# Kernel optimization log

Measured on AMD Instinct MI355X. Metric: run time of the kernel, lower is better.

The kernel has to match this reference:

```python
import jax, jax.numpy as jnp
import numpy as np

N = 20000
E = 320000
F_IN = 50
HID = 64          # hidden_channels
HEADS = 8
WIDTH = HID * HEADS  # 512
NUM_CLASSES = 121


def setup_inputs() -> dict:
    key = jax.random.key(0)
    ks = jax.random.split(key, 16)
    def p(k, shape, fan_in):
        return (jax.random.normal(k, shape, dtype=jnp.float32) / np.sqrt(fan_in)).astype(jnp.float32)
    x = jax.random.normal(ks[0], (N, F_IN), dtype=jnp.float32)
    edge_index = jax.random.randint(ks[1], (2, E), 0, N, dtype=jnp.int64)
    return {
        "x": x,
        "edge_index": edge_index,
        # layer 1: 50 -> 64, heads=8, concat
        "W1": p(ks[2], (F_IN, HEADS * HID), F_IN),
        "a1_src": p(ks[3], (HEADS, HID), HID),
        "a1_dst": p(ks[4], (HEADS, HID), HID),
        "b1": jnp.zeros((HEADS * HID,), jnp.float32),
        # layer 2: 512 -> 512, heads=1, concat
        "W2": p(ks[5], (WIDTH, WIDTH), WIDTH),
        "a2_src": p(ks[6], (1, WIDTH), WIDTH),
        "a2_dst": p(ks[7], (1, WIDTH), WIDTH),
        "b2": jnp.zeros((WIDTH,), jnp.float32),
        # layer 3: 512 -> 121, heads=1, concat=False (mean)
        "W3": p(ks[8], (WIDTH, NUM_CLASSES), WIDTH),
        "a3_src": p(ks[9], (1, NUM_CLASSES), NUM_CLASSES),
        "a3_dst": p(ks[10], (1, NUM_CLASSES), NUM_CLASSES),
        "b3": jnp.zeros((NUM_CLASSES,), jnp.float32),
    }


def gat_conv(x, src, dst, W, a_src, a_dst, b, heads, out_ch, concat):
    n = x.shape[0]
    h = (x @ W).reshape(n, heads, out_ch)                 # [N, H, C]
    al_s = jnp.sum(h * a_src, axis=-1)                     # [N, H]
    al_d = jnp.sum(h * a_dst, axis=-1)                     # [N, H]
    e = jax.nn.leaky_relu(al_s[src] + al_d[dst], 0.2)      # [E, H]
    # edge softmax per destination node (stable)
    m = jax.ops.segment_max(e, dst, num_segments=n)        # [N, H]
    m = jnp.where(jnp.isfinite(m), m, 0.0)
    ex = jnp.exp(e - m[dst])
    z = jax.ops.segment_sum(ex, dst, num_segments=n)       # [N, H]
    alpha = ex / (z[dst] + 1e-16)                          # [E, H]
    msg = h[src] * alpha[..., None]                        # [E, H, C]
    out = jax.ops.segment_sum(msg, dst, num_segments=n)    # [N, H, C]
    out = out.reshape(n, heads * out_ch) if concat else out.mean(axis=1)
    return out + b


def reference(x, edge_index, W1, a1_src, a1_dst, b1, W2, a2_src, a2_dst, b2, W3, a3_src, a3_dst, b3):
    n = x.shape[0]
    # PyG GATConv adds self loops by default
    loops = jnp.arange(n, dtype=edge_index.dtype)
    src = jnp.concatenate([edge_index[0], loops])
    dst = jnp.concatenate([edge_index[1], loops])
    # eval mode: dropout is identity
    x1 = gat_conv(x, src, dst, W1, a1_src, a1_dst, b1, HEADS, HID, True)
    h = jax.nn.elu(x1)
    x1 = gat_conv(h, src, dst, W2, a2_src, a2_dst, b2, 1, WIDTH, True)
    h = jax.nn.elu(x1)
    x1 = gat_conv(h, src, dst, W3, a3_src, a3_dst, b3, 1, NUM_CLASSES, False)
    return x1
```

## Files before the change

### kernel.cpp

```cpp
#include <hip/hip_runtime.h>
#include <hip/hip_bf16.h>
#include <hip/hip_fp16.h>

#define NN     20000
#define ERAW   320000
#define ETOT   (ERAW + NN)
#define F_IN   50
#define HID    64
#define HEADS  8
#define WIDTH  512
#define NCLS   121
#define NCLS_P 128

typedef __attribute__((ext_vector_type(8))) __bf16 bf16x8;
typedef __attribute__((ext_vector_type(4))) float floatx4;

__device__ __forceinline__ unsigned short f32_to_bf16_rn(float f) {
  unsigned u = __float_as_uint(f);
  unsigned r = u + 0x7fffu + ((u >> 16) & 1u);
  return (unsigned short)(r >> 16);
}
__device__ __forceinline__ void split_one(float f, unsigned short& h,
                                          unsigned short& l) {
  h = f32_to_bf16_rn(f);
  float fh = __uint_as_float(((unsigned)h) << 16);
  l = f32_to_bf16_rn(f - fh);
}

__device__ __forceinline__ float2 u2f2(unsigned u) {
  __half2 hv = *reinterpret_cast<__half2*>(&u);
  return __half22float2(hv);
}

__device__ __forceinline__ void gll16(const unsigned short* g,
                                      const unsigned short* l) {
  __builtin_amdgcn_global_load_lds(
      (const __attribute__((address_space(1))) unsigned int*)(const void*)g,
      (__attribute__((address_space(3))) unsigned int*)(void*)l, 16, 0, 0);
}

#define PW_BLOCKS 449
__global__ __launch_bounds__(256) void prep_weights(
    const float* __restrict__ W1, const float* __restrict__ W2,
    const float* __restrict__ W3, const float* __restrict__ a1s,
    const float* __restrict__ a1d, unsigned short* __restrict__ w1hHi,
    unsigned short* __restrict__ w1hLo, unsigned short* __restrict__ w2tHi,
    unsigned short* __restrict__ w2tLo, unsigned short* __restrict__ w3tHi,
    unsigned short* __restrict__ w3tLo, float* __restrict__ w1as,
    float* __restrict__ w1ad) {
  __shared__ float t[32][33];
  const int b = blockIdx.x;
  if (b < 320) {
    const float* W;
    unsigned short *thi, *tlo;
    int M, Mp, bx, by;
    const int K = WIDTH;
    if (b < 256) {
      W = W2; thi = w2tHi; tlo = w2tLo; M = WIDTH; Mp = WIDTH;
      bx = b & 15; by = b >> 4;
    } else {
      int bb = b - 256;
      W = W3; thi = w3tHi; tlo = w3tLo; M = NCLS; Mp = NCLS_P;
      bx = bb & 15; by = bb >> 4;
    }
    int k0 = bx * 32, m0 = by * 32;
    int tx = threadIdx.x & 31, ty = threadIdx.x >> 5;
    #pragma unroll
    for (int r = 0; r < 4; ++r) {
      int k = k0 + ty + r * 8, m = m0 + tx;
      float v = 0.f;
      if (k < K && m < M) v = W[(size_t)k * M + m];
      t[ty + r * 8][tx] = v;
    }
    __syncthreads();
    #pragma unroll
    for (int r = 0; r < 4; ++r) {
      int m = m0 + ty + r * 8, k = k0 + tx;
      if (m < Mp && k < K) {
        unsigned short h, l;
        split_one(t[tx][ty + r * 8], h, l);
        thi[(size_t)m * K + k] = h;
        tlo[(size_t)m * K + k] = l;
      }
    }
  } else if (b < 448) {
    int idx = (b - 320) * 256 + threadIdx.x;
    if (idx < HEADS * HID * HID) {
      int hd = idx >> 12, rem = idx & 4095;
      int col = rem >> 6, k = rem & 63;
      float v = (k < F_IN) ? W1[(size_t)k * WIDTH + hd * HID + col] : 0.f;
      unsigned short h, l;
      split_one(v, h, l);
      w1hHi[idx] = h;
      w1hLo[idx] = l;
    }
  } else {
    for (int idx = threadIdx.x; idx < 2 * F_IN * HEADS; idx += 256) {
      int which = idx >= F_IN * HEADS;
      int r = which ? idx - F_IN * HEADS : idx;
      int k = r >> 3, h = r & 7;
      const float* a = which ? a1d : a1s;
      float s = 0.f;
      for (int c = 0; c < HID; ++c)
        s += W1[(size_t)k * WIDTH + h * HID + c] * a[h * HID + c];
      (which ? w1ad : w1as)[r] = s;
    }
  }
}

template <int MI>
__global__ __launch_bounds__(512) void gemm_split_db(
    const unsigned short* __restrict__ Ahi, const unsigned short* __restrict__ Alo,
    const unsigned short* __restrict__ Bthi, const unsigned short* __restrict__ Btlo,
    __half* __restrict__ C16, int N, int K, int M, int Mp, int RB, int CB) {
  constexpr int ABUF = MI * 2048;
  constexpr int BHALF = MI * 4096;
  constexpr int BUF = MI * 4096 + 16384;
  constexpr int NGW = (MI * 8 + 32) / 8;
  __shared__ unsigned short lds[2 * BUF];

  const int f = blockIdx.x;
  const int xcd = f & 7;
  const int g = f >> 3;
  const int cb = g % CB;
  const int rb = (g / CB) * 8 + xcd;
  if (rb >= RB) return;
  const int r0 = rb * (MI * 32), c0 = cb * 128;

  const int tid = threadIdx.x;
  const int wave = tid >> 6, lane = tid & 63;
  const int wr = wave >> 2, wc = wave & 3;
  const int lkg = lane >> 4, lmn = lane & 15;

  const int row8 = lane >> 3, cslot = lane & 7;
  const unsigned short* gsrc[NGW];
  int ldsoff[NGW];
  #pragma unroll
  for (int i = 0; i < NGW; ++i) {
    int q = wave * NGW + i;
    int a, rg;
    if (q < MI * 4)      { a = 0; rg = q; }
    else if (q < MI * 8) { a = 1; rg = q - MI * 4; }
    else { int qb = q - MI * 8; a = 2 + (qb >> 4); rg = qb & 15; }
    int r = rg * 8 + row8;
    int c = cslot ^ (r & 7);
    const unsigned short* base =
        (a == 0) ? Ahi : (a == 1) ? Alo : (a == 2) ? Bthi : Btlo;
    size_t grow;
    if (a < 2) {
      int ra = r0 + r;
      if (ra > N - 1) ra = N - 1;
      grow = (size_t)ra;
    } else {
      grow = (size_t)(c0 + r);
    }
    gsrc[i] = base + grow * K + c * 8;
    int aoff = (a == 0) ? 0 : (a == 1) ? ABUF : (a == 2) ? BHALF
                                              : (BHALF + 8192);
    ldsoff[i] = aoff + rg * 512;
  }

  int rowA[MI], m7A[MI], rowB[2], m7B[2];
  #pragma unroll
  for (int mi = 0; mi < MI; ++mi) {
    int m = wr * (MI * 16) + mi * 16 + lmn;
    rowA[mi] = m * 64;  m7A[mi] = m & 7;
  }
  #pragma unroll
  for (int ni = 0; ni < 2; ++ni) {
    int n = wc * 32 + ni * 16 + lmn;
    rowB[ni] = BHALF + n * 64;  m7B[ni] = n & 7;
  }

  floatx4 acc[MI][2] = {};

  #pragma unroll
  for (int i = 0; i < NGW; ++i) gll16(gsrc[i], lds + ldsoff[i]);

  const int nk = K >> 6;
  for (int t = 0; t < nk; ++t) {
    if (t + 1 < nk) {
      const unsigned short* dst = lds + ((t + 1) & 1) * BUF;
      #pragma unroll
      for (int i = 0; i < NGW; ++i)
        gll16(gsrc[i] + (t + 1) * 64, dst + ldsoff[i]);
      if constexpr (MI == 4) {
        asm volatile("s_waitcnt vmcnt(8)" ::: "memory");
      } else {
        asm volatile("s_waitcnt vmcnt(6)" ::: "memory");
      }
    } else {
      asm volatile("s_waitcnt vmcnt(0)" ::: "memory");
    }
    __builtin_amdgcn_sched_barrier(0);
    __builtin_amdgcn_s_barrier();
    __builtin_amdgcn_sched_barrier(0);

    const unsigned short* Lb = lds + (t & 1) * BUF;
    #pragma unroll
    for (int ksub = 0; ksub < 2; ++ksub) {
      bf16x8 fAhi[MI], fAlo[MI], fBhi[2], fBlo[2];
      #pragma unroll
      for (int mi = 0; mi < MI; ++mi) {
        int s = rowA[mi] + (((ksub << 2) | lkg) ^ m7A[mi]) * 8;
        fAhi[mi] = *(const bf16x8*)(Lb + s);
        fAlo[mi] = *(const bf16x8*)(Lb + s + ABUF);
      }
      #pragma unroll
      for (int ni = 0; ni < 2; ++ni) {
        int s = rowB[ni] + (((ksub << 2) | lkg) ^ m7B[ni]) * 8;
        fBhi[ni] = *(const bf16x8*)(Lb + s);
        fBlo[ni] = *(const bf16x8*)(Lb + s + 8192);
      }
      #pragma unroll
      for (int mi = 0; mi < MI; ++mi)
        #pragma unroll
        for (int ni = 0; ni < 2; ++ni) {
          acc[mi][ni] = __builtin_amdgcn_mfma_f32_16x16x32_bf16(
              fAhi[mi], fBhi[ni], acc[mi][ni], 0, 0, 0);
          acc[mi][ni] = __builtin_amdgcn_mfma_f32_16x16x32_bf16(
              fAhi[mi], fBlo[ni], acc[mi][ni], 0, 0, 0);
          acc[mi][ni] = __builtin_amdgcn_mfma_f32_16x16x32_bf16(
              fAlo[mi], fBhi[ni], acc[mi][ni], 0, 0, 0);
        }
    }

    __builtin_amdgcn_sched_barrier(0);
    asm volatile("s_waitcnt lgkmcnt(0)" ::: "memory");
    __builtin_amdgcn_s_barrier();
    __builtin_amdgcn_sched_barrier(0);
  }

  #pragma unroll
  for (int mi = 0; mi < MI; ++mi) {
    #pragma unroll
    for (int r = 0; r < 4; ++r) {
      int grow = r0 + wr * (MI * 16) + mi * 16 + lkg * 4 + r;
      if (grow >= N) continue;
      #pragma unroll
      for (int ni = 0; ni < 2; ++ni) {
        int gcol = c0 + wc * 32 + ni * 16 + lmn;
        float v = (gcol < M) ? acc[mi][ni][r] : 0.f;
        C16[(size_t)grow * Mp + gcol] = __float2half(v);
      }
    }
  }
}

__global__ __launch_bounds__(256) void gemm_l1_heads(
    const unsigned short* __restrict__ Ahi, const unsigned short* __restrict__ Alo,
    const unsigned short* __restrict__ Bthi, const unsigned short* __restrict__ Btlo,
    unsigned short* __restrict__ outHi, unsigned short* __restrict__ outLo,
    const float* __restrict__ bias) {
  __shared__ unsigned short sAhi[8192], sAlo[8192], sBhi[4096], sBlo[4096];
  const int tid = threadIdx.x;
  const int wave = tid >> 6, lane = tid & 63;
  const int r0 = blockIdx.x * 128;
  const int hd = blockIdx.y;
  const int lkg = lane >> 4, lmn = lane & 15;

  #pragma unroll
  for (int t = 0; t < 4; ++t) {
    int cid = tid + t * 256;
    int row = cid >> 3, c = cid & 7;
    int gr = r0 + row; if (gr > NN - 1) gr = NN - 1;
    const size_t goff = (size_t)gr * WIDTH + hd * HID + c * 8;
    int loff = (((c >> 2) * 4 + (c & 3)) * 128 + row) * 8;
    *(uint4*)(sAhi + loff) = *(const uint4*)(Ahi + goff);
    *(uint4*)(sAlo + loff) = *(const uint4*)(Alo + goff);
  }
  #pragma unroll
  for (int t = 0; t < 2; ++t) {
    int cid = tid + t * 256;
    int col = cid >> 3, c = cid & 7;
    const size_t goff = (size_t)(hd * HID + col) * HID + c * 8;
    int loff = (((c >> 2) * 4 + (c & 3)) * 64 + col) * 8;
    *(uint4*)(sBhi + loff) = *(const uint4*)(Bthi + goff);
    *(uint4*)(sBlo + loff) = *(const uint4*)(Btlo + goff);
  }
  __syncthreads();

  floatx4 acc[2][4] = {};
  #pragma unroll
  for (int ks = 0; ks < 2; ++ks) {
    bf16x8 fAhi[2], fAlo[2], fBhi[4], fBlo[4];
    #pragma unroll
    for (int mi = 0; mi < 2; ++mi) {
      int m = wave * 32 + mi * 16 + lmn;
      int off = ((ks * 4 + lkg) * 128 + m) * 8;
      fAhi[mi] = *(const bf16x8*)(sAhi + off);
      fAlo[mi] = *(const bf16x8*)(sAlo + off);
    }
    #pragma unroll
    for (int ni = 0; ni < 4; ++ni) {
      int n = ni * 16 + lmn;
      int off = ((ks * 4 + lkg) * 64 + n) * 8;
      fBhi[ni] = *(const bf16x8*)(sBhi + off);
      fBlo[ni] = *(const bf16x8*)(sBlo + off);
    }
    #pragma unroll
    for (int mi = 0; mi < 2; ++mi)
      #pragma unroll
      for (int ni = 0; ni < 4; ++ni) {
        acc[mi][ni] = __builtin_amdgcn_mfma_f32_16x16x32_bf16(
            fAhi[mi], fBhi[ni], acc[mi][ni], 0, 0, 0);
        acc[mi][ni] = __builtin_amdgcn_mfma_f32_16x16x32_bf16(
            fAhi[mi], fBlo[ni], acc[mi][ni], 0, 0, 0);
        acc[mi][ni] = __builtin_amdgcn_mfma_f32_16x16x32_bf16(
            fAlo[mi], fBhi[ni], acc[mi][ni], 0, 0, 0);
      }
  }

  #pragma unroll
  for (int mi = 0; mi < 2; ++mi) {
    #pragma unroll
    for (int r = 0; r < 4; ++r) {
      int grow = r0 + wave * 32 + mi * 16 + (lane >> 4) * 4 + r;
      if (grow >= NN) continue;
      #pragma unroll
      for (int ni = 0; ni < 4; ++ni) {
        int gcol = hd * HID + ni * 16 + lmn;
        float v = acc[mi][ni][r] + bias[gcol];
        v = (v > 0.f) ? v : (__expf(v) - 1.0f);
        unsigned short hh, ll;
        split_one(v, hh, ll);
        outHi[(size_t)grow * WIDTH + gcol] = hh;
        outLo[(size_t)grow * WIDTH + gcol] = ll;
      }
    }
  }
}

__global__ __launch_bounds__(256) void al1_kernel(
    const float* __restrict__ x, const float* __restrict__ w1as,
    const float* __restrict__ w1ad, float* __restrict__ al_s,
    float* __restrict__ al_d) {
  int n = (blockIdx.x * blockDim.x + threadIdx.x) >> 6;
  int lane = threadIdx.x & 63;
  if (n >= NN) return;
  float xv = (lane < F_IN) ? x[(size_t)n * F_IN + lane] : 0.f;
  float ws[HEADS], wd[HEADS];
  #pragma unroll
  for (int h = 0; h < HEADS; ++h) {
    ws[h] = (lane < F_IN) ? w1as[lane * HEADS + h] : 0.f;
    wd[h] = (lane < F_IN) ? w1ad[lane * HEADS + h] : 0.f;
  }
  #pragma unroll
  for (int h = 0; h < HEADS; ++h) {
    float ss = xv * ws[h], sd = xv * wd[h];
    #pragma unroll
    for (int o = 32; o; o >>= 1) {
      ss += __shfl_xor(ss, o);
      sd += __shfl_xor(sd, o);
    }
    if (lane == 0) {
      al_s[n * HEADS + h] = ss;
      al_d[n * HEADS + h] = sd;
    }
  }
}

template <int C, int CS>
__global__ __launch_bounds__(256) void compute_al16(
    const __half* __restrict__ h16, const float* __restrict__ a_src,
    const float* __restrict__ a_dst, float* __restrict__ al_s,
    float* __restrict__ al_d) {
  int n = (blockIdx.x * blockDim.x + threadIdx.x) >> 6;
  int lane = threadIdx.x & 63;
  if (n >= NN) return;
  const __half* hr = h16 + (size_t)n * CS;
  float ss = 0.f, sd = 0.f;
  if (C % 512 == 0) {
    uint4 raw = *(const uint4*)(hr + lane * 8);
    float f[8];
    float2 t;
    t = u2f2(raw.x); f[0] = t.x; f[1] = t.y;
    t = u2f2(raw.y); f[2] = t.x; f[3] = t.y;
    t = u2f2(raw.z); f[4] = t.x; f[5] = t.y;
    t = u2f2(raw.w); f[6] = t.x; f[7] = t.y;
    #pragma unroll
    for (int j = 0; j < 8; ++j) {
      int c = lane * 8 + j;
      ss += f[j] * a_src[c];
      sd += f[j] * a_dst[c];
    }
  } else {
    for (int c = lane; c < C; c += 64) {
      float v = __half2float(hr[c]);
      ss += v * a_src[c];
      sd += v * a_dst[c];
    }
  }
  #pragma unroll
  for (int o = 32; o; o >>= 1) {
    ss += __shfl_xor(ss, o);
    sd += __shfl_xor(sd, o);
  }
  if (lane == 0) {
    al_s[n] = ss;
    al_d[n] = sd;
  }
}

__global__ __launch_bounds__(256) void count_deg(
    const int* __restrict__ edst, int* __restrict__ deg) {
  int e = blockIdx.x * blockDim.x + threadIdx.x;
  if (e >= ETOT) return;
  int d = (e < ERAW) ? edst[e] : (e - ERAW);
  atomicAdd(&deg[d], 1);
}

__global__ __launch_bounds__(1024) void scan_deg(
    const int* __restrict__ deg, int* __restrict__ rowptr) {
  __shared__ int part[1024];
  const int t = threadIdx.x;
  const int CHUNK = (NN + 1023) / 1024;
  int lo = t * CHUNK, hi = min(lo + CHUNK, NN);
  int s = 0;
  for (int i = lo; i < hi; ++i) s += deg[i];
  part[t] = s;
  __syncthreads();
  for (int off = 1; off < 1024; off <<= 1) {
    int v = (t >= off) ? part[t - off] : 0;
    __syncthreads();
    part[t] += v;
    __syncthreads();
  }
  int base = (t == 0) ? 0 : part[t - 1];
  for (int i = lo; i < hi; ++i) {
    rowptr[i] = base;
    base += deg[i];
  }
  if (t == 1023) rowptr[NN] = part[1023];
}

__global__ __launch_bounds__(256) void scatter_csr(
    const int* __restrict__ esrc, const int* __restrict__ edst,
    const int* __restrict__ rowptr, int* __restrict__ cnt,
    int* __restrict__ csrc) {
  int e = blockIdx.x * blockDim.x + threadIdx.x;
  if (e >= ETOT) return;
  int s, d;
  if (e < ERAW) { s = esrc[e]; d = edst[e]; }
  else          { s = e - ERAW; d = e - ERAW; }
  int pos = rowptr[d] + atomicAdd(&cnt[d], 1);
  csrc[pos] = s;
}

__global__ __launch_bounds__(256) void agg_x_sm(
    const int* __restrict__ rowptr, const int* __restrict__ csrc,
    const float* __restrict__ al_s, const float* __restrict__ al_d,
    const float* __restrict__ x, unsigned short* __restrict__ outHi,
    unsigned short* __restrict__ outLo) {
  const int w = threadIdx.x >> 6, lane = threadIdx.x & 63;
  const int d = blockIdx.x * 4 + w;
  if (d >= NN) return;
  const int r0 = rowptr[d], r1 = rowptr[d + 1];
  const int mh = lane & 7;
  const float ald_my = al_d[d * HEADS + mh];
  float m_my = al_s[d * HEADS + mh] + ald_my;
  m_my = (m_my > 0.f) ? m_my : 0.2f * m_my;

  float z_my = 0.f;
  float acc[HEADS];
  #pragma unroll
  for (int hh = 0; hh < HEADS; ++hh) acc[hh] = 0.f;

  int p = r0;
  for (; p + 8 <= r1; p += 8) {
    int s[8];
    #pragma unroll
    for (int j = 0; j < 8; ++j) s[j] = csrc[p + j];
    float xv[8];
    #pragma unroll
    for (int j = 0; j < 8; ++j)
      xv[j] = (lane < F_IN) ? x[(size_t)s[j] * F_IN + lane] : 0.f;
    float av[8];
    #pragma unroll
    for (int j = 0; j < 8; ++j) av[j] = al_s[s[j] * HEADS + mh];
    #pragma unroll
    for (int j = 0; j < 8; ++j) {
      float v = av[j] + ald_my;
      v = (v > 0.f) ? v : 0.2f * v;
      float a = __expf(v - m_my);
      z_my += a;
      #pragma unroll
      for (int hh = 0; hh < HEADS; ++hh) acc[hh] += __shfl(a, hh, 8) * xv[j];
    }
  }
  for (; p < r1; ++p) {
    int s = csrc[p];
    float v = al_s[s * HEADS + mh] + ald_my;
    v = (v > 0.f) ? v : 0.2f * v;
    float a = __expf(v - m_my);
    z_my += a;
    float xv = (lane < F_IN) ? x[(size_t)s * F_IN + lane] : 0.f;
    #pragma unroll
    for (int hh = 0; hh < HEADS; ++hh) acc[hh] += __shfl(a, hh, 8) * xv;
  }

  #pragma unroll
  for (int hh = 0; hh < HEADS; ++hh) {
    float zh = __shfl(z_my, hh, 8);
    float v = (lane < F_IN) ? acc[hh] / (zh + 1e-16f) : 0.f;
    unsigned short h2, l2;
    split_one(v, h2, l2);
    outHi[(size_t)d * WIDTH + hh * HID + lane] = h2;
    outLo[(size_t)d * WIDTH + hh * HID + lane] = l2;
  }
}

__global__ __launch_bounds__(256) void pull_agg_w(
    const int* __restrict__ rowptr, const int* __restrict__ csrc,
    const float* __restrict__ al_s, const float* __restrict__ al_d,
    const __half* __restrict__ h16, const float* __restrict__ bias,
    unsigned short* __restrict__ outHi, unsigned short* __restrict__ outLo) {
  const int w = threadIdx.x >> 6;
  const int lane = threadIdx.x & 63;
  const int d = blockIdx.x * 4 + w;
  if (d >= NN) return;
  const int r0 = rowptr[d], r1 = rowptr[d + 1];
  const float ald = al_d[d];
  float m = al_s[d] + ald;
  m = (m > 0.f) ? m : 0.2f * m;

  const int base = lane * 8;
  const __half* hb = h16 + base;
  float acc[8];
  #pragma unroll
  for (int j = 0; j < 8; ++j) acc[j] = 0.f;
  float z = 0.f;

  int p = r0;
  for (; p + 8 <= r1; p += 8) {
    int s[8];
    #pragma unroll
    for (int j = 0; j < 8; ++j) s[j] = csrc[p + j];
    uint4 raw8[8];
    #pragma unroll
    for (int j = 0; j < 8; ++j)
      raw8[j] = *(const uint4*)(hb + (size_t)s[j] * WIDTH);
    float av[8];
    #pragma unroll
    for (int j = 0; j < 8; ++j) av[j] = al_s[s[j]];
    #pragma unroll
    for (int j = 0; j < 8; ++j) {
      float v = av[j] + ald;
      v = (v > 0.f) ? v : 0.2f * v;
      float a = __expf(v - m);
      z += a;
      float2 f0 = u2f2(raw8[j].x), f1 = u2f2(raw8[j].y);
      float2 f2 = u2f2(raw8[j].z), f3 = u2f2(raw8[j].w);
      acc[0] += f0.x * a; acc[1] += f0.y * a;
      acc[2] += f1.x * a; acc[3] += f1.y * a;
      acc[4] += f2.x * a; acc[5] += f2.y * a;
      acc[6] += f3.x * a; acc[7] += f3.y * a;
    }
  }
  for (; p < r1; ++p) {
    int s = csrc[p];
    float v = al_s[s] + ald;
    v = (v > 0.f) ? v : 0.2f * v;
    float a = __expf(v - m);
    z += a;
    uint4 raw = *(const uint4*)(hb + (size_t)s * WIDTH);
    float2 f0 = u2f2(raw.x), f1 = u2f2(raw.y);
    float2 f2 = u2f2(raw.z), f3 = u2f2(raw.w);
    acc[0] += f0.x * a; acc[1] += f0.y * a;
    acc[2] += f1.x * a; acc[3] += f1.y * a;
    acc[4] += f2.x * a; acc[5] += f2.y * a;
    acc[6] += f3.x * a; acc[7] += f3.y * a;
  }
  const float iz = 1.0f / (z + 1e-16f);

  #pragma unroll
  for (int j = 0; j < 8; ++j) {
    float v = acc[j] * iz + bias[base + j];
    v = (v > 0.f) ? v : (__expf(v) - 1.0f);
    unsigned short hh, ll;
    split_one(v, hh, ll);
    outHi[(size_t)d * WIDTH + base + j] = hh;
    outLo[(size_t)d * WIDTH + base + j] = ll;
  }
}

__global__ __launch_bounds__(256) void pull_agg_n(
    const int* __restrict__ rowptr, const int* __restrict__ csrc,
    const float* __restrict__ al_s, const float* __restrict__ al_d,
    const __half* __restrict__ h16, const float* __restrict__ bias,
    float* __restrict__ out) {
  const int w = threadIdx.x >> 6, lane = threadIdx.x & 63;
  const int half = lane >> 5, li = lane & 31;
  const int d = blockIdx.x * 8 + w * 2 + half;
  if (d >= NN) return;
  const int r0 = rowptr[d], r1 = rowptr[d + 1];
  const float ald = al_d[d];
  float m = al_s[d] + ald;
  m = (m > 0.f) ? m : 0.2f * m;

  const int base = li * 4;
  const __half* hb = h16 + base;
  float acc[4] = {0.f, 0.f, 0.f, 0.f};
  float z = 0.f;

  for (int p = r0; p < r1; p += 8) {
    int s[8];
    #pragma unroll
    for (int j = 0; j < 8; ++j) {
      int pj = p + j; if (pj > r1 - 1) pj = r1 - 1;
      s[j] = csrc[pj];
    }
    uint2 raw[8];
    #pragma unroll
    for (int j = 0; j < 8; ++j)
      raw[j] = *(const uint2*)(hb + (size_t)s[j] * NCLS_P);
    float av[8];
    #pragma unroll
    for (int j = 0; j < 8; ++j) av[j] = al_s[s[j]];
    #pragma unroll
    for (int j = 0; j < 8; ++j) {
      float v = av[j] + ald;
      v = (v > 0.f) ? v : 0.2f * v;
      float a = __expf(v - m);
      if (p + j >= r1) a = 0.f;
      z += a;
      float2 f0 = u2f2(raw[j].x), f1 = u2f2(raw[j].y);
      acc[0] += f0.x * a; acc[1] += f0.y * a;
      acc[2] += f1.x * a; acc[3] += f1.y * a;
    }
  }
  const float iz = 1.0f / (z + 1e-16f);

  #pragma unroll
  for (int j = 0; j < 4; ++j) {
    int col = base + j;
    if (col < NCLS)
      out[(size_t)d * NCLS + col] = acc[j] * iz + bias[col];
  }
}

extern "C" void kernel_launch(void* const* d_in, const int* in_sizes, int n_in,
                              void* d_out, int out_size, void* d_ws,
                              size_t ws_size, hipStream_t stream) {
  const float* x      = (const float*)d_in[0];
  const int*   ei     = (const int*)d_in[1];
  const float* W1     = (const float*)d_in[2];
  const float* a1_src = (const float*)d_in[3];
  const float* a1_dst = (const float*)d_in[4];
  const float* b1     = (const float*)d_in[5];
  const float* W2     = (const float*)d_in[6];
  const float* a2_src = (const float*)d_in[7];
  const float* a2_dst = (const float*)d_in[8];
  const float* b2     = (const float*)d_in[9];
  const float* W3     = (const float*)d_in[10];
  const float* a3_src = (const float*)d_in[11];
  const float* a3_dst = (const float*)d_in[12];
  const float* b3     = (const float*)d_in[13];
  float* out = (float*)d_out;

  const int* esrc = ei;
  const int* edst = ei + ERAW;

  unsigned short* p1Hi  = (unsigned short*)d_ws;
  unsigned short* p1Lo  = p1Hi + (size_t)NN * WIDTH;
  unsigned short* p2Hi  = p1Lo + (size_t)NN * WIDTH;
  unsigned short* p2Lo  = p2Hi + (size_t)NN * WIDTH;
  __half*        h16    = (__half*)(p2Lo + (size_t)NN * WIDTH);
  unsigned short* w1hHi = (unsigned short*)(h16 + (size_t)NN * WIDTH);
  unsigned short* w1hLo = w1hHi + (size_t)HEADS * HID * HID;
  unsigned short* w2tHi = w1hLo + (size_t)HEADS * HID * HID;
  unsigned short* w2tLo = w2tHi + (size_t)WIDTH * WIDTH;
  unsigned short* w3tHi = w2tLo + (size_t)WIDTH * WIDTH;
  unsigned short* w3tLo = w3tHi + (size_t)NCLS_P * WIDTH;
  float* al_s   = (float*)(w3tLo + (size_t)NCLS_P * WIDTH);
  float* al_d   = al_s + (size_t)NN * HEADS;
  float* w1as   = al_d + (size_t)NN * HEADS;
  float* w1ad   = w1as + F_IN * HEADS;
  int* deg      = (int*)(w1ad + F_IN * HEADS);
  int* cnt      = deg + NN;
  int* rowptr   = cnt + NN;
  int* csrc     = rowptr + NN + 4;

  hipMemsetAsync(deg, 0, (size_t)(2 * NN) * sizeof(int), stream);
  const int eblk = (ETOT + 255) / 256;
  count_deg<<<eblk, 256, 0, stream>>>(edst, deg);
  scan_deg<<<1, 1024, 0, stream>>>(deg, rowptr);
  scatter_csr<<<eblk, 256, 0, stream>>>(esrc, edst, rowptr, cnt, csrc);

  prep_weights<<<PW_BLOCKS, 256, 0, stream>>>(
      W1, W2, W3, a1_src, a1_dst, w1hHi, w1hLo, w2tHi, w2tLo, w3tHi, w3tLo,
      w1as, w1ad);

  const int nwblk = (NN + 3) / 4;

  al1_kernel<<<nwblk, 256, 0, stream>>>(x, w1as, w1ad, al_s, al_d);
  agg_x_sm<<<nwblk, 256, 0, stream>>>(rowptr, csrc, al_s, al_d, x, p1Hi,
                                      p1Lo);
  gemm_l1_heads<<<dim3((NN + 127) / 128, HEADS), 256, 0, stream>>>(
      p1Hi, p1Lo, w1hHi, w1hLo, p2Hi, p2Lo, b1);

  const int RB2 = (NN + 127) / 128;
  const int G2 = ((RB2 + 7) / 8) * 8 * (WIDTH / 128);
  gemm_split_db<4><<<G2, 512, 0, stream>>>(
      p2Hi, p2Lo, w2tHi, w2tLo, h16, NN, WIDTH, WIDTH, WIDTH, RB2,
      WIDTH / 128);
  compute_al16<WIDTH, WIDTH><<<nwblk, 256, 0, stream>>>(h16, a2_src, a2_dst,
                                                        al_s, al_d);
  pull_agg_w<<<nwblk, 256, 0, stream>>>(rowptr, csrc, al_s, al_d, h16, b2,
                                        p1Hi, p1Lo);

  const int RB3 = (NN + 63) / 64;
  const int G3 = ((RB3 + 7) / 8) * 8 * (NCLS_P / 128);
  gemm_split_db<2><<<G3, 512, 0, stream>>>(
      p1Hi, p1Lo, w3tHi, w3tLo, h16, NN, WIDTH, NCLS, NCLS_P, RB3,
      NCLS_P / 128);
  compute_al16<NCLS, NCLS_P><<<nwblk, 256, 0, stream>>>(h16, a3_src, a3_dst,
                                                        al_s, al_d);
  pull_agg_n<<<(NN + 7) / 8, 256, 0, stream>>>(rowptr, csrc, al_s, al_d, h16,
                                               b3, out);
}
```

Before: 390.2 us.

## Stage only hi bf16 halves in LDS; load lo halves directly from global

The split-bf16 GEMM now stages only the high halves of A and B in shared memory, halving the LDS footprint and the number of global-to-LDS copies per K step. The low halves are read straight from global memory into registers inside the MFMA loop. Launch bounds now request 4 blocks per SM to raise occupancy from the smaller LDS use. The risk is that the direct global loads of the lo fragments sit on the critical path of the inner loop with no double-buffering. Those loads are also less coalesced than the staged path.

Result: slower. 438.5 us (+12.4%).

```diff
diff --git a/kernel.cpp b/kernel.cpp
--- a/kernel.cpp
+++ b/kernel.cpp
@@ -109,14 +109,13 @@
 }
 
 template <int MI>
-__global__ __launch_bounds__(512) void gemm_split_db(
+__global__ __launch_bounds__(512, 4) void gemm_split_db(
     const unsigned short* __restrict__ Ahi, const unsigned short* __restrict__ Alo,
     const unsigned short* __restrict__ Bthi, const unsigned short* __restrict__ Btlo,
     __half* __restrict__ C16, int N, int K, int M, int Mp, int RB, int CB) {
   constexpr int ABUF = MI * 2048;
-  constexpr int BHALF = MI * 4096;
-  constexpr int BUF = MI * 4096 + 16384;
-  constexpr int NGW = (MI * 8 + 32) / 8;
+  constexpr int BUF = MI * 2048 + 8192;
+  constexpr int NGW = (MI * 4 + 16) / 8;
   __shared__ unsigned short lds[2 * BUF];
 
   const int f = blockIdx.x;
@@ -138,16 +137,13 @@
   #pragma unroll
   for (int i = 0; i < NGW; ++i) {
     int q = wave * NGW + i;
-    int a, rg;
-    if (q < MI * 4)      { a = 0; rg = q; }
-    else if (q < MI * 8) { a = 1; rg = q - MI * 4; }
-    else { int qb = q - MI * 8; a = 2 + (qb >> 4); rg = qb & 15; }
+    int a = (q < MI * 4) ? 0 : 1;
+    int rg = (a == 0) ? q : q - MI * 4;
     int r = rg * 8 + row8;
     int c = cslot ^ (r & 7);
-    const unsigned short* base =
-        (a == 0) ? Ahi : (a == 1) ? Alo : (a == 2) ? Bthi : Btlo;
+    const unsigned short* base = a ? Bthi : Ahi;
     size_t grow;
-    if (a < 2) {
+    if (a == 0) {
       int ra = r0 + r;
       if (ra > N - 1) ra = N - 1;
       grow = (size_t)ra;
@@ -155,21 +151,24 @@
       grow = (size_t)(c0 + r);
     }
     gsrc[i] = base + grow * K + c * 8;
-    int aoff = (a == 0) ? 0 : (a == 1) ? ABUF : (a == 2) ? BHALF
-                                              : (BHALF + 8192);
-    ldsoff[i] = aoff + rg * 512;
+    ldsoff[i] = (a ? ABUF : 0) + rg * 512;
   }
 
   int rowA[MI], m7A[MI], rowB[2], m7B[2];
+  const unsigned short* loA[MI];
+  const unsigned short* loB[2];
   #pragma unroll
   for (int mi = 0; mi < MI; ++mi) {
     int m = wr * (MI * 16) + mi * 16 + lmn;
     rowA[mi] = m * 64;  m7A[mi] = m & 7;
+    int ra = r0 + m; if (ra > N - 1) ra = N - 1;
+    loA[mi] = Alo + (size_t)ra * K + lkg * 8;
   }
   #pragma unroll
   for (int ni = 0; ni < 2; ++ni) {
     int n = wc * 32 + ni * 16 + lmn;
-    rowB[ni] = BHALF + n * 64;  m7B[ni] = n & 7;
+    rowB[ni] = ABUF + n * 64;  m7B[ni] = n & 7;
+    loB[ni] = Btlo + (size_t)(c0 + n) * K + lkg * 8;
   }
 
   floatx4 acc[MI][2] = {};
@@ -185,9 +184,9 @@
       for (int i = 0; i < NGW; ++i)
         gll16(gsrc[i] + (t + 1) * 64, dst + ldsoff[i]);
       if constexpr (MI == 4) {
-        asm volatile("s_waitcnt vmcnt(8)" ::: "memory");
+        asm volatile("s_waitcnt vmcnt(4)" ::: "memory");
       } else {
-        asm volatile("s_waitcnt vmcnt(6)" ::: "memory");
+        asm volatile("s_waitcnt vmcnt(3)" ::: "memory");
       }
     } else {
       asm volatile("s_waitcnt vmcnt(0)" ::: "memory");
@@ -197,6 +196,7 @@
     __builtin_amdgcn_sched_barrier(0);
 
     const unsigned short* Lb = lds + (t & 1) * BUF;
+    const int kofs = t * 64;
     #pragma unroll
     for (int ksub = 0; ksub < 2; ++ksub) {
       bf16x8 fAhi[MI], fAlo[MI], fBhi[2], fBlo[2];
@@ -204,13 +204,13 @@
       for (int mi = 0; mi < MI; ++mi) {
         int s = rowA[mi] + (((ksub << 2) | lkg) ^ m7A[mi]) * 8;
         fAhi[mi] = *(const bf16x8*)(Lb + s);
-        fAlo[mi] = *(const bf16x8*)(Lb + s + ABUF);
+        fAlo[mi] = *(const bf16x8*)(loA[mi] + kofs + ksub * 32);
       }
       #pragma unroll
       for (int ni = 0; ni < 2; ++ni) {
         int s = rowB[ni] + (((ksub << 2) | lkg) ^ m7B[ni]) * 8;
         fBhi[ni] = *(const bf16x8*)(Lb + s);
-        fBlo[ni] = *(const bf16x8*)(Lb + s + 8192);
+        fBlo[ni] = *(const bf16x8*)(loB[ni] + kofs + ksub * 32);
       }
       #pragma unroll
       for (int mi = 0; mi < MI; ++mi)
```
